# Optimization experiments

Measured on AMD Instinct MI355X. Metric: run time of the kernel, lower is better.

Reference implementation:

```python
import jax, jax.numpy as jnp
import numpy as np

D_MODEL = 512
HEADS = 8
HEAD_DIM = D_MODEL // HEADS
LN_EPS = 1e-5


def _rel_shift(pos_score):
    # pos_score: [B, H, T, P] with P = 2T-1
    B, H, T, P = pos_score.shape
    padded = jnp.pad(pos_score, ((0, 0), (0, 0), (0, 0), (1, 0)))  # [B,H,T,P+1]
    shifted = padded.reshape(B, H, P + 1, T)[:, :, 1:, :].reshape(B, H, T, P)
    return shifted[:, :, :, : P // 2 + 1]  # [B,H,T,T]


def setup_inputs() -> dict:
    key = jax.random.key(0)
    ks = jax.random.split(key, 16)
    B, T = 16, 512
    P = 2 * T - 1
    s = 1.0 / np.sqrt(D_MODEL)
    inp = {
        "x": jax.random.normal(ks[0], (B, T, D_MODEL), jnp.float32),
        "pos_emb": jax.random.normal(ks[1], (B, P, D_MODEL), jnp.float32),
        "ln_g": jnp.ones((D_MODEL,), jnp.float32),
        "ln_b": jnp.zeros((D_MODEL,), jnp.float32),
        "Wq": jax.random.normal(ks[2], (D_MODEL, D_MODEL), jnp.float32) * s,
        "bq": jnp.zeros((D_MODEL,), jnp.float32),
        "Wk": jax.random.normal(ks[3], (D_MODEL, D_MODEL), jnp.float32) * s,
        "bk": jnp.zeros((D_MODEL,), jnp.float32),
        "Wv": jax.random.normal(ks[4], (D_MODEL, D_MODEL), jnp.float32) * s,
        "bv": jnp.zeros((D_MODEL,), jnp.float32),
        "Wp": jax.random.normal(ks[5], (D_MODEL, D_MODEL), jnp.float32) * s,
        "bp": jnp.zeros((D_MODEL,), jnp.float32),
        "content_bias": jax.random.normal(ks[6], (HEADS, HEAD_DIM), jnp.float32) * 0.05,
        "position_bias": jax.random.normal(ks[7], (HEADS, HEAD_DIM), jnp.float32) * 0.05,
        "Wo": jax.random.normal(ks[8], (D_MODEL, D_MODEL), jnp.float32) * s,
        "bo": jnp.zeros((D_MODEL,), jnp.float32),
    }
    return inp


def reference(x, pos_emb, ln_g, ln_b, Wq, bq, Wk, bk, Wv, bv, Wp, bp,
              content_bias, position_bias, Wo, bo):
    B, T, D = x.shape
    H, hd = HEADS, HEAD_DIM

    # LayerNorm over last dim
    mu = jnp.mean(x, axis=-1, keepdims=True)
    var = jnp.var(x, axis=-1, keepdims=True)
    xn = (x - mu) / jnp.sqrt(var + LN_EPS) * ln_g + ln_b

    q = (xn @ Wq.T + bq).reshape(B, T, H, hd)                 # [B,T,H,hd]
    k = (xn @ Wk.T + bk).reshape(B, T, H, hd)                 # [B,T,H,hd]
    v = (xn @ Wv.T + bv).reshape(B, T, H, hd)                 # [B,T,H,hd]
    p = (pos_emb @ Wp.T + bp).reshape(B, -1, H, hd)           # [B,P,H,hd]

    content_score = jnp.einsum('bshd,bthd->bhst', q + content_bias, k)   # [B,H,T,T]
    pos_score = jnp.einsum('bshd,bphd->bhsp', q + position_bias, p)      # [B,H,T,P]
    pos_score = _rel_shift(pos_score)                                    # [B,H,T,T]

    scores = (content_score + pos_score) / jnp.sqrt(jnp.asarray(hd, x.dtype))
    w = jax.nn.softmax(scores, axis=-1)
    ctx = jnp.einsum('bhst,bthd->bshd', w, v).reshape(B, T, D)
    return ctx @ Wo.T + bo
```

## Files before the change

### kernel.cpp

```cpp
#include <hip/hip_runtime.h>
#include <cstdio>
#include <cstdint>


typedef short s16x8 __attribute__((ext_vector_type(8)));
typedef float f32x4 __attribute__((ext_vector_type(4)));
typedef unsigned short u16x4 __attribute__((ext_vector_type(4)));
typedef unsigned short u16x8 __attribute__((ext_vector_type(8)));

#define CSCALE 0.1803368801111204f

#if __has_builtin(__builtin_amdgcn_exp2f)
#define EXP2(x) __builtin_amdgcn_exp2f(x)
#else
#define EXP2(x) exp2f(x)
#endif

__device__ __forceinline__ unsigned short f2bf(float f) {
  unsigned int u = __builtin_bit_cast(unsigned int, f);
  unsigned int r = (u + 0x7FFFu + ((u >> 16) & 1u)) >> 16;
  return (unsigned short)r;
}
__device__ __forceinline__ float bf2f(unsigned short h) {
  unsigned int u = ((unsigned int)h) << 16;
  return __builtin_bit_cast(float, u);
}
__device__ __forceinline__ size_t pk(int row, int col) {
  return (size_t)(row >> 4) * 8192 + (col >> 5) * 512 + ((col >> 3) & 3) * 128 +
         (row & 15) * 8 + (col & 7);
}

__device__ __forceinline__ void gload_lds16(const unsigned short* g,
                                            unsigned short* l) {
  __builtin_amdgcn_global_load_lds(
      (const __attribute__((address_space(1))) unsigned int*)g,
      (__attribute__((address_space(3))) unsigned int*)l, 16, 0, 0);
}

__global__ __launch_bounds__(256) void megaprep(
    const float* __restrict__ x, const float* __restrict__ g,
    const float* __restrict__ bb, unsigned short* __restrict__ xpk,
    const float* __restrict__ pe, unsigned short* __restrict__ pepk,
    const float* __restrict__ Wq, const float* __restrict__ Wk,
    const float* __restrict__ Wp, const float* __restrict__ Wv,
    const float* __restrict__ Wo, const float* __restrict__ bq,
    const float* __restrict__ bk, unsigned short* __restrict__ wqk,
    unsigned short* __restrict__ wpm, unsigned short* __restrict__ wvm,
    unsigned short* __restrict__ wom, float* __restrict__ bqk) {
  const int bid = blockIdx.x, tid = threadIdx.x;
  if (bid < 2048) {
    const int wave = tid >> 6, lane = tid & 63;
    const int row = bid * 4 + wave;
    const int c0 = lane * 8;
    const float* xr = x + (size_t)row * 512 + c0;
    float4 v0 = *(const float4*)xr;
    float4 v1 = *(const float4*)(xr + 4);
    float vv[8] = {v0.x, v0.y, v0.z, v0.w, v1.x, v1.y, v1.z, v1.w};
    float s = 0.f, ss = 0.f;
#pragma unroll
    for (int j = 0; j < 8; ++j) { s += vv[j]; ss += vv[j] * vv[j]; }
#pragma unroll
    for (int d = 1; d < 64; d <<= 1) {
      s += __shfl_xor(s, d, 64);
      ss += __shfl_xor(ss, d, 64);
    }
    const float mu = s * (1.0f / 512.0f);
    const float var = ss * (1.0f / 512.0f) - mu * mu;
    const float rstd = rsqrtf(var + 1e-5f);
    u16x8 o;
#pragma unroll
    for (int j = 0; j < 8; ++j)
      o[j] = f2bf((vv[j] - mu) * rstd * g[c0 + j] + bb[c0 + j]);
    *(u16x8*)(xpk + pk(row, c0)) = o;
  } else if (bid < 6144) {
    int gid = (bid - 2048) * 256 + tid;
    int e = gid * 8;
    int r = e >> 9, c = e & 511;
    int b = r >> 10, u = r & 1023;
    u16x8 o = {0, 0, 0, 0, 0, 0, 0, 0};
    if (u < 1023) {
      const float* src = pe + (size_t)(b * 1023 + u) * 512 + c;
      float4 v0 = *(const float4*)src;
      float4 v1 = *(const float4*)(src + 4);
      o[0] = f2bf(v0.x); o[1] = f2bf(v0.y); o[2] = f2bf(v0.z); o[3] = f2bf(v0.w);
      o[4] = f2bf(v1.x); o[5] = f2bf(v1.y); o[6] = f2bf(v1.z); o[7] = f2bf(v1.w);
    }
    *(u16x8*)(pepk + (size_t)b * 524288 + pk(u, c)) = o;
  } else {
    int gid = (bid - 6144) * 256 + tid;
    int idx = gid * 8;
    int region = idx >> 18, off = idx & 262143;
    const float* src = (region == 0)   ? Wq
                       : (region == 1) ? Wk
                       : (region == 2) ? Wp
                       : (region == 3) ? Wv
                                       : Wo;
    float4 v0 = *(const float4*)(src + off);
    float4 v1 = *(const float4*)(src + off + 4);
    u16x8 o;
    o[0] = f2bf(v0.x); o[1] = f2bf(v0.y); o[2] = f2bf(v0.z); o[3] = f2bf(v0.w);
    o[4] = f2bf(v1.x); o[5] = f2bf(v1.y); o[6] = f2bf(v1.z); o[7] = f2bf(v1.w);
    int n = off >> 9, k = off & 511;
    unsigned short* dst;
    int nrow = n;
    if (region == 0) { dst = wqk; }
    else if (region == 1) { dst = wqk; nrow = n + 512; }
    else if (region == 2) { dst = wpm; }
    else if (region == 3) { dst = wvm; }
    else { dst = wom; }
    *(u16x8*)(dst + pk(nrow, k)) = o;
    if (idx < 1024) {
#pragma unroll
      for (int j = 0; j < 8; j++) {
        int ii = idx + j;
        bqk[ii] = (ii < 512) ? bq[ii] : bk[ii - 512];
      }
    }
  }
}

template <bool SWAP>
__device__ __forceinline__ void gemm128_db(
    const unsigned short* __restrict__ Apk, int astrip8,
    const unsigned short* __restrict__ Bpk, int bstrip8,
    unsigned short* __restrict__ lA, unsigned short* __restrict__ lB,
    int wave, int lane, f32x4 acc[4][4]) {
  const int wr = wave >> 1, wc = wave & 1;
  const unsigned short* ga =
      Apk + (size_t)(astrip8 + 2 * wave) * 8192 + lane * 8;
  const unsigned short* gb =
      Bpk + (size_t)(bstrip8 + 2 * wave) * 8192 + lane * 8;
#define STG(ks, buf)                                                         \
  _Pragma("unroll") for (int s = 0; s < 2; ++s) {                            \
    _Pragma("unroll") for (int hf = 0; hf < 2; ++hf) {                       \
      gload_lds16(ga + (size_t)s * 8192 + (ks) * 1024 + hf * 512,            \
                  lA + (buf) * 8192 + (2 * wave + s) * 1024 + hf * 512);     \
      gload_lds16(gb + (size_t)s * 8192 + (ks) * 1024 + hf * 512,            \
                  lB + (buf) * 8192 + (2 * wave + s) * 1024 + hf * 512);     \
    }                                                                        \
  }
  STG(0, 0);
  __syncthreads();
  const unsigned short* lar = lA + (wr * 4) * 1024 + lane * 8;
  const unsigned short* lbr = lB + (wc * 4) * 1024 + lane * 8;
#pragma unroll
  for (int ks = 0; ks < 8; ++ks) {
    const int cur = ks & 1;
    if (ks < 7) { STG(ks + 1, cur ^ 1); }
#pragma unroll
    for (int kk = 0; kk < 2; ++kk) {
      s16x8 af[4], bf[4];
#pragma unroll
      for (int mt = 0; mt < 4; ++mt)
        af[mt] = *(const s16x8*)(lar + cur * 8192 + mt * 1024 + kk * 512);
#pragma unroll
      for (int nt = 0; nt < 4; ++nt)
        bf[nt] = *(const s16x8*)(lbr + cur * 8192 + nt * 1024 + kk * 512);
#pragma unroll
      for (int mt = 0; mt < 4; ++mt)
#pragma unroll
        for (int nt = 0; nt < 4; ++nt)
          acc[mt][nt] =
              SWAP ? __builtin_amdgcn_mfma_f32_16x16x32_bf16(
                         bf[nt], af[mt], acc[mt][nt], 0, 0, 0)
                   : __builtin_amdgcn_mfma_f32_16x16x32_bf16(
                         af[mt], bf[nt], acc[mt][nt], 0, 0, 0);
    }
    __syncthreads();
  }
#undef STG
}

__global__ __launch_bounds__(256) void proj_all(
    const unsigned short* __restrict__ xpk, const unsigned short* __restrict__ pepk,
    const unsigned short* __restrict__ wqk, const unsigned short* __restrict__ wpm,
    const unsigned short* __restrict__ wvm, const float* __restrict__ bqk,
    const float* __restrict__ bp, const float* __restrict__ bv,
    const float* __restrict__ cbv, const float* __restrict__ pbv,
    unsigned short* __restrict__ qc, unsigned short* __restrict__ qp,
    unsigned short* __restrict__ kb, unsigned short* __restrict__ pbuf,
    unsigned short* __restrict__ vth) {
  __shared__ __align__(16) unsigned short lA[16384];
  __shared__ __align__(16) unsigned short lB[16384];
  const int tid = threadIdx.x, lane = tid & 63, wave = tid >> 6;
  int bid = blockIdx.x;
  bid = (bid & 7) * 160 + (bid >> 3);
  const int wr = wave >> 1, wc = wave & 1;
  const int fr = lane & 15, hi2 = lane >> 4;
  f32x4 fz = {0.f, 0.f, 0.f, 0.f};
  f32x4 acc[4][4];
#pragma unroll
  for (int i = 0; i < 4; i++)
#pragma unroll
    for (int j = 0; j < 4; j++) acc[i][j] = fz;

  if (bid < 512) {
    int m_t = bid >> 3, n_t = bid & 7;
    gemm128_db<true>(xpk, m_t * 8, wqk, n_t * 8, lA, lB, wave, lane, acc);
    int m0 = m_t * 128 + wr * 64, n0 = n_t * 128 + wc * 64;
#pragma unroll
    for (int nt = 0; nt < 4; ++nt) {
      int colb = n0 + nt * 16 + hi2 * 4;
      float4 b4 = *(const float4*)(bqk + colb);
      float bvv[4] = {b4.x, b4.y, b4.z, b4.w};
      if (colb < 512) {
        int h = colb >> 6, cc = colb & 63;
        float4 c4 = *(const float4*)(cbv + colb);
        float4 p4 = *(const float4*)(pbv + colb);
        float cvv[4] = {c4.x, c4.y, c4.z, c4.w};
        float pvv[4] = {p4.x, p4.y, p4.z, p4.w};
        size_t cpart = (size_t)(cc >> 5) * 512 + ((cc & 31) >> 3) * 128 +
                       (cc & 7) + (size_t)h * 32768;
#pragma unroll
        for (int mt = 0; mt < 4; ++mt) {
          int row = m0 + mt * 16 + fr;
          int b = row >> 9, s16i = (row & 511) >> 4;
          size_t idx = ((size_t)b * 8 * 32 + s16i) * 1024 + cpart + fr * 8;
          u16x4 oc, op;
#pragma unroll
          for (int r = 0; r < 4; ++r) {
            float val = acc[mt][nt][r] + bvv[r];
            oc[r] = f2bf((val + cvv[r]) * CSCALE);
            op[r] = f2bf((val + pvv[r]) * CSCALE);
          }
          *(u16x4*)(qc + idx) = oc;
          *(u16x4*)(qp + idx) = op;
        }
      } else {
        int c2 = colb - 512, h = c2 >> 6, cc = c2 & 63;
        size_t cpart = (size_t)(cc >> 5) * 512 + ((cc & 31) >> 3) * 128 +
                       (cc & 7) + (size_t)h * 32768;
#pragma unroll
        for (int mt = 0; mt < 4; ++mt) {
          int row = m0 + mt * 16 + fr;
          int b = row >> 9, s16i = (row & 511) >> 4;
          size_t idx = ((size_t)b * 8 * 32 + s16i) * 1024 + cpart + fr * 8;
          u16x4 ok;
#pragma unroll
          for (int r = 0; r < 4; ++r) ok[r] = f2bf(acc[mt][nt][r] + bvv[r]);
          *(u16x4*)(kb + idx) = ok;
        }
      }
    }
  } else if (bid < 1024) {
    int pid = bid - 512;
    int b = pid >> 5, rem = pid & 31;
    int m_tb = rem >> 2, n_t = rem & 3;
    gemm128_db<true>(pepk + (size_t)b * 524288, m_tb * 8, wpm, n_t * 8, lA,
                     lB, wave, lane, acc);
    int u0 = m_tb * 128 + wr * 64, n0 = n_t * 128 + wc * 64;
#pragma unroll
    for (int nt = 0; nt < 4; ++nt) {
      int colb = n0 + nt * 16 + hi2 * 4;
      float4 b4 = *(const float4*)(bp + colb);
      float bvv[4] = {b4.x, b4.y, b4.z, b4.w};
      int h = colb >> 6, cc = colb & 63;
      size_t cbase = (size_t)(b * 8 + h) * 65536 + (cc >> 5) * 512 +
                     ((cc & 31) >> 3) * 128 + (cc & 7);
#pragma unroll
      for (int mt = 0; mt < 4; ++mt) {
        int u = u0 + mt * 16 + fr;
        size_t idx = cbase + (size_t)(u >> 4) * 1024 + (u & 15) * 8;
        u16x4 o;
        if (u >= 1023) {
          o[0] = 0; o[1] = 0; o[2] = 0; o[3] = 0;
        } else {
#pragma unroll
          for (int r = 0; r < 4; ++r) o[r] = f2bf(acc[mt][nt][r] + bvv[r]);
        }
        *(u16x4*)(pbuf + idx) = o;
      }
    }
  } else {
    int vid = bid - 1024;
    int m_t = vid >> 2, n_t = vid & 3;
    gemm128_db<false>(xpk, m_t * 8, wvm, n_t * 8, lA, lB, wave, lane, acc);
    int m0 = m_t * 128 + wr * 64, n0 = n_t * 128 + wc * 64;
#pragma unroll
    for (int nt = 0; nt < 4; ++nt) {
      int col = n0 + nt * 16 + fr;
      float bval = bv[col];
      int h = col >> 6, d = col & 63;
#pragma unroll
      for (int mt = 0; mt < 4; ++mt) {
        int rowb = m0 + mt * 16 + hi2 * 4;
        int b = rowb >> 9, t = rowb & 511;
        size_t idx =
            ((size_t)((b * 8 + h) * 4 + (d >> 4)) * 16 + (t >> 5)) * 512 +
            ((t & 31) >> 3) * 128 + (d & 15) * 8 + (t & 7);
        u16x4 hv;
#pragma unroll
        for (int r = 0; r < 4; ++r) hv[r] = f2bf(acc[mt][nt][r] + bval);
        *(u16x4*)(vth + idx) = hv;
      }
    }
  }
}

__global__ __launch_bounds__(256) void out_gemm(
    const unsigned short* __restrict__ ctxpk, const unsigned short* __restrict__ wom,
    const float* __restrict__ bo, float* __restrict__ out) {
  __shared__ __align__(16) unsigned short lA[16384];
  __shared__ __align__(16) unsigned short lB[16384];
  const int tid = threadIdx.x, lane = tid & 63, wave = tid >> 6;
  const int bid = blockIdx.x;
  const int wr = wave >> 1, wc = wave & 1;
  const int fr = lane & 15, hi2 = lane >> 4;
  int m_t = bid >> 2, n_t = bid & 3;
  f32x4 fz = {0.f, 0.f, 0.f, 0.f};
  f32x4 acc[4][4];
#pragma unroll
  for (int i = 0; i < 4; i++)
#pragma unroll
    for (int j = 0; j < 4; j++) acc[i][j] = fz;
  gemm128_db<true>(ctxpk, m_t * 8, wom, n_t * 8, lA, lB, wave, lane, acc);
  int m0 = m_t * 128 + wr * 64, n0 = n_t * 128 + wc * 64;
#pragma unroll
  for (int nt = 0; nt < 4; ++nt) {
    int colb = n0 + nt * 16 + hi2 * 4;
    float4 b4 = *(const float4*)(bo + colb);
#pragma unroll
    for (int mt = 0; mt < 4; ++mt) {
      int row = m0 + mt * 16 + fr;
      float4 o;
      o.x = acc[mt][nt][0] + b4.x;
      o.y = acc[mt][nt][1] + b4.y;
      o.z = acc[mt][nt][2] + b4.z;
      o.w = acc[mt][nt][3] + b4.w;
      *(float4*)(out + (size_t)row * 512 + colb) = o;
    }
  }
}

__global__ __launch_bounds__(256) void flash_attn(
    const unsigned short* __restrict__ qc, const unsigned short* __restrict__ qp,
    const unsigned short* __restrict__ kb, const unsigned short* __restrict__ pm,
    const unsigned short* __restrict__ vth, unsigned short* __restrict__ ctxpk) {
  const int id = blockIdx.x;
  const int bh = id & 127, b = bh >> 3, h = bh & 7;
  const int s_blk = id >> 7;
  const int tid = threadIdx.x, wave = tid >> 6, lane = tid & 63;
  const int fr = lane & 15, hi2 = lane >> 4, fc = hi2 * 8;
  const int s0w = s_blk * 64 + wave * 16;
  const int crow = hi2 * 4;

  __shared__ __align__(16) unsigned short Ph_s[4][16][40];
  unsigned short(*Phw)[40] = Ph_s[wave];

  int srcl[4];
#pragma unroll
  for (int r = 0; r < 4; ++r) srcl[r] = (hi2 << 4) | ((fr - (crow + r) - 1) & 15);

  const size_t qtb = ((size_t)(b * 8 + h) * 32 + (s0w >> 4)) * 1024 + lane * 8;
  s16x8 aqc0 = *(const s16x8*)(qc + qtb);
  s16x8 aqc1 = *(const s16x8*)(qc + qtb + 512);
  s16x8 aqp0 = *(const s16x8*)(qp + qtb);
  s16x8 aqp1 = *(const s16x8*)(qp + qtb + 512);

  const unsigned short* kpk = kb + (size_t)(b * 8 + h) * 32 * 1024 + lane * 8;
  const unsigned short* ppk = pm + (size_t)(b * 8 + h) * 64 * 1024 + lane * 8;
  const unsigned short* vhk = vth + (size_t)(b * 8 + h) * 64 * 512 + lane * 8;

  f32x4 fz = {0.f, 0.f, 0.f, 0.f};
  f32x4 Oacc[4] = {fz, fz, fz, fz};
  float lsum[4] = {0.f, 0.f, 0.f, 0.f};

  s16x8 kfA[4], pfA[6], vfA[4], kfB[4], pfB[6], vfB[4];

#define LOADF(step, kf, pf, vf)                                              \
  {                                                                          \
    const int t0_ = (step) * 32;                                             \
    const int u0w_ = t0_ - s0w + 496;                                        \
    const int kt_ = t0_ >> 4, ut_ = u0w_ >> 4, vt_ = t0_ >> 5;               \
    _Pragma("unroll") for (int nt = 0; nt < 2; ++nt) {                       \
      const unsigned short* kr = kpk + (size_t)(kt_ + nt) * 1024;            \
      kf[2 * nt] = *(const s16x8*)kr;                                        \
      kf[2 * nt + 1] = *(const s16x8*)(kr + 512);                            \
    }                                                                        \
    _Pragma("unroll") for (int nt = 0; nt < 3; ++nt) {                       \
      const unsigned short* pr = ppk + (size_t)(ut_ + nt) * 1024;            \
      pf[2 * nt] = *(const s16x8*)pr;                                        \
      pf[2 * nt + 1] = *(const s16x8*)(pr + 512);                            \
    }                                                                        \
    _Pragma("unroll") for (int nt = 0; nt < 4; ++nt)                         \
        vf[nt] = *(const s16x8*)(vhk + (size_t)(nt * 16 + vt_) * 512);       \
  }

#define STEPF(kf, pf, vf)                                                    \
  {                                                                          \
    f32x4 sc[2] = {fz, fz};                                                  \
    __builtin_amdgcn_s_setprio(1);                                           \
    _Pragma("unroll") for (int nt = 0; nt < 2; ++nt) {                       \
      sc[nt] = __builtin_amdgcn_mfma_f32_16x16x32_bf16(aqc0, kf[2 * nt],     \
                                                       sc[nt], 0, 0, 0);     \
      sc[nt] = __builtin_amdgcn_mfma_f32_16x16x32_bf16(aqc1, kf[2 * nt + 1], \
                                                       sc[nt], 0, 0, 0);     \
    }                                                                        \
    f32x4 sp[3];                                                             \
    _Pragma("unroll") for (int nt = 0; nt < 3; ++nt) {                       \
      f32x4 t = fz;                                                          \
      t = __builtin_amdgcn_mfma_f32_16x16x32_bf16(aqp0, pf[2 * nt], t, 0, 0, 0); \
      t = __builtin_amdgcn_mfma_f32_16x16x32_bf16(aqp1, pf[2 * nt + 1], t, 0, 0, 0); \
      sp[nt] = t;                                                            \
    }                                                                        \
    __builtin_amdgcn_s_setprio(0);                                           \
    float sj[3][4];                                                          \
    _Pragma("unroll") for (int j = 0; j < 3; ++j)                            \
        _Pragma("unroll") for (int r = 0; r < 4; ++r)                        \
        sj[j][r] = __shfl(sp[j][r], srcl[r], 64);                            \
    _Pragma("unroll") for (int nt = 0; nt < 2; ++nt) {                       \
      int tc = nt * 16 + fr;                                                 \
      _Pragma("unroll") for (int r = 0; r < 4; ++r) {                        \
        float pos = (fr <= crow + r) ? sj[nt][r] : sj[nt + 1][r];            \
        float e = EXP2(sc[nt][r] + pos);                                     \
        lsum[r] += e;                                                        \
        Phw[crow + r][tc] = f2bf(e);                                         \
      }                                                                      \
    }                                                                        \
    s16x8 ah = *(const s16x8*)&Phw[fr][fc];                                  \
    __builtin_amdgcn_s_setprio(1);                                           \
    _Pragma("unroll") for (int nt = 0; nt < 4; ++nt)                         \
        Oacc[nt] = __builtin_amdgcn_mfma_f32_16x16x32_bf16(ah, vf[nt],       \
                                                           Oacc[nt], 0, 0, 0); \
    __builtin_amdgcn_s_setprio(0);                                           \
  }

  LOADF(0, kfA, pfA, vfA);
  for (int s2 = 0; s2 < 8; ++s2) {
    LOADF(2 * s2 + 1, kfB, pfB, vfB);
    STEPF(kfA, pfA, vfA);
    if (s2 < 7) LOADF(2 * s2 + 2, kfA, pfA, vfA);
    STEPF(kfB, pfB, vfB);
  }
#undef LOADF
#undef STEPF

#pragma unroll
  for (int d = 1; d < 16; d <<= 1)
#pragma unroll
    for (int r = 0; r < 4; ++r) lsum[r] += __shfl_xor(lsum[r], d, 64);
#pragma unroll
  for (int nt = 0; nt < 4; ++nt)
#pragma unroll
    for (int r = 0; r < 4; ++r) {
      float o = Oacc[nt][r] / lsum[r];
      int row = b * 512 + s0w + crow + r;
      int col = h * 64 + nt * 16 + fr;
      ctxpk[pk(row, col)] = f2bf(o);
    }
}

extern "C" void kernel_launch(void* const* d_in, const int* in_sizes, int n_in,
                              void* d_out, int out_size, void* d_ws,
                              size_t ws_size, hipStream_t stream) {
  const float* x = (const float*)d_in[0];
  const float* pe = (const float*)d_in[1];
  const float* ln_g = (const float*)d_in[2];
  const float* ln_b = (const float*)d_in[3];
  const float* Wq = (const float*)d_in[4];
  const float* bq = (const float*)d_in[5];
  const float* Wk = (const float*)d_in[6];
  const float* bk = (const float*)d_in[7];
  const float* Wv = (const float*)d_in[8];
  const float* bv = (const float*)d_in[9];
  const float* Wp = (const float*)d_in[10];
  const float* bp = (const float*)d_in[11];
  const float* cb = (const float*)d_in[12];
  const float* pb = (const float*)d_in[13];
  const float* Wo = (const float*)d_in[14];
  const float* bo = (const float*)d_in[15];
  float* out = (float*)d_out;

  char* ws = (char*)d_ws;
  size_t off = 0;
  auto alloc = [&](size_t bytes) -> char* {
    char* ptr = ws + off;
    off = (off + bytes + 255) & ~(size_t)255;
    return ptr;
  };
  unsigned short* xpk = (unsigned short*)alloc((size_t)8192 * 512 * 2);
  unsigned short* ctxpk = xpk;
  unsigned short* pepk = (unsigned short*)alloc((size_t)16384 * 512 * 2);
  unsigned short* vt_hi = (unsigned short*)alloc((size_t)8192 * 512 * 2);
  unsigned short* wqk = (unsigned short*)alloc((size_t)1024 * 512 * 2);
  unsigned short* wpm = (unsigned short*)alloc((size_t)512 * 512 * 2);
  unsigned short* wvm = (unsigned short*)alloc((size_t)512 * 512 * 2);
  unsigned short* wom = (unsigned short*)alloc((size_t)512 * 512 * 2);
  float* bqk = (float*)alloc(1024 * 4);
  unsigned short* qc = (unsigned short*)alloc((size_t)8192 * 512 * 2);
  unsigned short* qp = (unsigned short*)alloc((size_t)8192 * 512 * 2);
  unsigned short* kbuf = (unsigned short*)alloc((size_t)8192 * 512 * 2);
  unsigned short* pbuf = (unsigned short*)alloc((size_t)16384 * 512 * 2);

  if (ws_size < off) {
    fprintf(stderr, "kernel_launch: ws too small (need %zu, have %zu)\n", off,
            ws_size);
    return;
  }

  megaprep<<<6784, 256, 0, stream>>>(x, ln_g, ln_b, xpk, pe, pepk, Wq, Wk, Wp,
                                     Wv, Wo, bq, bk, wqk, wpm, wvm, wom, bqk);
  proj_all<<<1280, 256, 0, stream>>>(xpk, pepk, wqk, wpm, wvm, bqk, bp, bv,
                                     cb, pb, qc, qp, kbuf, pbuf, vt_hi);
  flash_attn<<<1024, 256, 0, stream>>>(qc, qp, kbuf, pbuf, vt_hi, ctxpk);
  out_gemm<<<256, 256, 0, stream>>>(ctxpk, wom, bo, out);
}
```

Before: 215.8 us.

## Stage K, V and positional tiles through shared memory with async LDS loads

Each wave used to fetch its own K, V and positional fragments from global memory into registers. Now the four waves of a block split the job: one wave loads K, one loads V and two load P tiles, all straight into double-buffered shared memory through direct global-to-LDS loads. P uses an 8-slot ring buffer, so the positional tiles that overlap between the waves' diagonals are fetched once per block. This cuts redundant global and L2 traffic but adds a __syncthreads per step and LDS read traffic.

```diff
diff --git a/kernel.cpp b/kernel.cpp
--- a/kernel.cpp
+++ b/kernel.cpp
@@ -343,7 +343,11 @@
   const int fr = lane & 15, hi2 = lane >> 4, fc = hi2 * 8;
   const int s0w = s_blk * 64 + wave * 16;
   const int crow = hi2 * 4;
-
+  const int pbase0 = 31 - 4 * s_blk;
+
+  __shared__ __align__(16) unsigned short lK[4096];
+  __shared__ __align__(16) unsigned short lV[4096];
+  __shared__ __align__(16) unsigned short lP[8192];
   __shared__ __align__(16) unsigned short Ph_s[4][16][40];
   unsigned short(*Phw)[40] = Ph_s[wave];
 
@@ -357,83 +361,118 @@
   s16x8 aqp0 = *(const s16x8*)(qp + qtb);
   s16x8 aqp1 = *(const s16x8*)(qp + qtb + 512);
 
-  const unsigned short* kpk = kb + (size_t)(b * 8 + h) * 32 * 1024 + lane * 8;
-  const unsigned short* ppk = pm + (size_t)(b * 8 + h) * 64 * 1024 + lane * 8;
-  const unsigned short* vhk = vth + (size_t)(b * 8 + h) * 64 * 512 + lane * 8;
+  const unsigned short* kpk = kb + (size_t)(b * 8 + h) * 32768 + lane * 8;
+  const unsigned short* ppk = pm + (size_t)(b * 8 + h) * 65536 + lane * 8;
+  const unsigned short* vhk = vth + (size_t)(b * 8 + h) * 32768 + lane * 8;
+
+  if (wave == 0) {
+#pragma unroll
+    for (int c = 0; c < 4; ++c) gload_lds16(kpk + c * 512, lK + c * 512);
+  } else if (wave == 1) {
+#pragma unroll
+    for (int c = 0; c < 4; ++c)
+      gload_lds16(vhk + (size_t)(c * 16) * 512, lV + c * 512);
+  } else {
+#pragma unroll
+    for (int j = 0; j < 3; ++j) {
+      const int t = pbase0 - 3 + (wave - 2) * 3 + j;
+#pragma unroll
+      for (int hf = 0; hf < 2; ++hf)
+        gload_lds16(ppk + (size_t)t * 1024 + hf * 512,
+                    lP + (t & 7) * 1024 + hf * 512);
+    }
+  }
 
   f32x4 fz = {0.f, 0.f, 0.f, 0.f};
   f32x4 Oacc[4] = {fz, fz, fz, fz};
   float lsum[4] = {0.f, 0.f, 0.f, 0.f};
 
-  s16x8 kfA[4], pfA[6], vfA[4], kfB[4], pfB[6], vfB[4];
-
-#define LOADF(step, kf, pf, vf)                                              \
-  {                                                                          \
-    const int t0_ = (step) * 32;                                             \
-    const int u0w_ = t0_ - s0w + 496;                                        \
-    const int kt_ = t0_ >> 4, ut_ = u0w_ >> 4, vt_ = t0_ >> 5;               \
-    _Pragma("unroll") for (int nt = 0; nt < 2; ++nt) {                       \
-      const unsigned short* kr = kpk + (size_t)(kt_ + nt) * 1024;            \
-      kf[2 * nt] = *(const s16x8*)kr;                                        \
-      kf[2 * nt + 1] = *(const s16x8*)(kr + 512);                            \
-    }                                                                        \
-    _Pragma("unroll") for (int nt = 0; nt < 3; ++nt) {                       \
-      const unsigned short* pr = ppk + (size_t)(ut_ + nt) * 1024;            \
-      pf[2 * nt] = *(const s16x8*)pr;                                        \
-      pf[2 * nt + 1] = *(const s16x8*)(pr + 512);                            \
-    }                                                                        \
-    _Pragma("unroll") for (int nt = 0; nt < 4; ++nt)                         \
-        vf[nt] = *(const s16x8*)(vhk + (size_t)(nt * 16 + vt_) * 512);       \
-  }
-
-#define STEPF(kf, pf, vf)                                                    \
-  {                                                                          \
-    f32x4 sc[2] = {fz, fz};                                                  \
-    __builtin_amdgcn_s_setprio(1);                                           \
-    _Pragma("unroll") for (int nt = 0; nt < 2; ++nt) {                       \
-      sc[nt] = __builtin_amdgcn_mfma_f32_16x16x32_bf16(aqc0, kf[2 * nt],     \
-                                                       sc[nt], 0, 0, 0);     \
-      sc[nt] = __builtin_amdgcn_mfma_f32_16x16x32_bf16(aqc1, kf[2 * nt + 1], \
-                                                       sc[nt], 0, 0, 0);     \
-    }                                                                        \
-    f32x4 sp[3];                                                             \
-    _Pragma("unroll") for (int nt = 0; nt < 3; ++nt) {                       \
-      f32x4 t = fz;                                                          \
-      t = __builtin_amdgcn_mfma_f32_16x16x32_bf16(aqp0, pf[2 * nt], t, 0, 0, 0); \
-      t = __builtin_amdgcn_mfma_f32_16x16x32_bf16(aqp1, pf[2 * nt + 1], t, 0, 0, 0); \
-      sp[nt] = t;                                                            \
-    }                                                                        \
-    __builtin_amdgcn_s_setprio(0);                                           \
-    float sj[3][4];                                                          \
-    _Pragma("unroll") for (int j = 0; j < 3; ++j)                            \
-        _Pragma("unroll") for (int r = 0; r < 4; ++r)                        \
-        sj[j][r] = __shfl(sp[j][r], srcl[r], 64);                            \
-    _Pragma("unroll") for (int nt = 0; nt < 2; ++nt) {                       \
-      int tc = nt * 16 + fr;                                                 \
-      _Pragma("unroll") for (int r = 0; r < 4; ++r) {                        \
-        float pos = (fr <= crow + r) ? sj[nt][r] : sj[nt + 1][r];            \
-        float e = EXP2(sc[nt][r] + pos);                                     \
-        lsum[r] += e;                                                        \
-        Phw[crow + r][tc] = f2bf(e);                                         \
-      }                                                                      \
-    }                                                                        \
-    s16x8 ah = *(const s16x8*)&Phw[fr][fc];                                  \
-    __builtin_amdgcn_s_setprio(1);                                           \
-    _Pragma("unroll") for (int nt = 0; nt < 4; ++nt)                         \
-        Oacc[nt] = __builtin_amdgcn_mfma_f32_16x16x32_bf16(ah, vf[nt],       \
-                                                           Oacc[nt], 0, 0, 0); \
-    __builtin_amdgcn_s_setprio(0);                                           \
-  }
-
-  LOADF(0, kfA, pfA, vfA);
-  for (int s2 = 0; s2 < 8; ++s2) {
-    LOADF(2 * s2 + 1, kfB, pfB, vfB);
-    STEPF(kfA, pfA, vfA);
-    if (s2 < 7) LOADF(2 * s2 + 2, kfA, pfA, vfA);
-    STEPF(kfB, pfB, vfB);
-  }
-#undef LOADF
-#undef STEPF
+  __syncthreads();
+
+#pragma unroll 2
+  for (int s = 0; s < 16; ++s) {
+    const int cur = s & 1, nxt = cur ^ 1;
+    if (s < 15) {
+      const int sn = s + 1;
+      if (wave == 0) {
+#pragma unroll
+        for (int c = 0; c < 4; ++c)
+          gload_lds16(kpk + (size_t)(2 * sn) * 1024 + c * 512,
+                      lK + nxt * 2048 + c * 512);
+      } else if (wave == 1) {
+#pragma unroll
+        for (int c = 0; c < 4; ++c)
+          gload_lds16(vhk + (size_t)(c * 16 + sn) * 512,
+                      lV + nxt * 2048 + c * 512);
+      } else {
+        const int t = pbase0 + 2 * s + 3 + (wave - 2);
+#pragma unroll
+        for (int hf = 0; hf < 2; ++hf)
+          gload_lds16(ppk + (size_t)t * 1024 + hf * 512,
+                      lP + (t & 7) * 1024 + hf * 512);
+      }
+    }
+    const unsigned short* lk = lK + cur * 2048 + lane * 8;
+    const unsigned short* lv = lV + cur * 2048 + lane * 8;
+    s16x8 kf[4], pf[6], vf[4];
+#pragma unroll
+    for (int nt = 0; nt < 2; ++nt) {
+      kf[2 * nt] = *(const s16x8*)(lk + nt * 1024);
+      kf[2 * nt + 1] = *(const s16x8*)(lk + nt * 1024 + 512);
+    }
+#pragma unroll
+    for (int nt = 0; nt < 3; ++nt) {
+      const int t = pbase0 + 2 * s - wave + nt;
+      const unsigned short* lp = lP + (t & 7) * 1024 + lane * 8;
+      pf[2 * nt] = *(const s16x8*)lp;
+      pf[2 * nt + 1] = *(const s16x8*)(lp + 512);
+    }
+#pragma unroll
+    for (int nt = 0; nt < 4; ++nt) vf[nt] = *(const s16x8*)(lv + nt * 512);
+
+    f32x4 sc[2] = {fz, fz};
+    __builtin_amdgcn_s_setprio(1);
+#pragma unroll
+    for (int nt = 0; nt < 2; ++nt) {
+      sc[nt] = __builtin_amdgcn_mfma_f32_16x16x32_bf16(aqc0, kf[2 * nt],
+                                                       sc[nt], 0, 0, 0);
+      sc[nt] = __builtin_amdgcn_mfma_f32_16x16x32_bf16(aqc1, kf[2 * nt + 1],
+                                                       sc[nt], 0, 0, 0);
+    }
+    f32x4 sp[3];
+#pragma unroll
+    for (int nt = 0; nt < 3; ++nt) {
+      f32x4 t2 = fz;
+      t2 = __builtin_amdgcn_mfma_f32_16x16x32_bf16(aqp0, pf[2 * nt], t2, 0, 0, 0);
+      t2 = __builtin_amdgcn_mfma_f32_16x16x32_bf16(aqp1, pf[2 * nt + 1], t2, 0, 0, 0);
+      sp[nt] = t2;
+    }
+    __builtin_amdgcn_s_setprio(0);
+    float sj[3][4];
+#pragma unroll
+    for (int j = 0; j < 3; ++j)
+#pragma unroll
+      for (int r = 0; r < 4; ++r) sj[j][r] = __shfl(sp[j][r], srcl[r], 64);
+#pragma unroll
+    for (int nt = 0; nt < 2; ++nt) {
+      int tc = nt * 16 + fr;
+#pragma unroll
+      for (int r = 0; r < 4; ++r) {
+        float pos = (fr <= crow + r) ? sj[nt][r] : sj[nt + 1][r];
+        float e = EXP2(sc[nt][r] + pos);
+        lsum[r] += e;
+        Phw[crow + r][tc] = f2bf(e);
+      }
+    }
+    s16x8 ah = *(const s16x8*)&Phw[fr][fc];
+    __builtin_amdgcn_s_setprio(1);
+#pragma unroll
+    for (int nt = 0; nt < 4; ++nt)
+      Oacc[nt] = __builtin_amdgcn_mfma_f32_16x16x32_bf16(ah, vf[nt], Oacc[nt],
+                                                         0, 0, 0);
+    __builtin_amdgcn_s_setprio(0);
+    __syncthreads();
+  }
 
 #pragma unroll
   for (int d = 1; d < 16; d <<= 1)
```

Result: faster. 209.8 us (-2.8%).
